# Optimization experiments

Measured on AMD Instinct MI355X. Metric: run time of the kernel, lower is better.

The kernel has to match this reference:

```python
import jax, jax.numpy as jnp
import numpy as np

N, C, H, W, NH = 2, 192, 256, 256, 6  # batch, channels, height, width, heads


def conv(x, w, groups=1):
    # NCHW conv, SAME padding, stride 1 (matches nn.Conv2d with padding=k//2)
    return jax.lax.conv_general_dilated(
        x, w, window_strides=(1, 1), padding='SAME',
        dimension_numbers=('NCHW', 'OIHW', 'NCHW'),
        feature_group_count=groups)


def setup_inputs() -> dict:
    key = jax.random.key(0)
    ks = jax.random.split(key, 5)
    x = jax.random.normal(ks[0], (N, C, H, W), jnp.float32)
    w1 = jax.random.normal(ks[1], (3 * C, C, 1, 1), jnp.float32) * 0.05   # 1x1 qkv proj
    w2 = jax.random.normal(ks[2], (3 * C, 1, 3, 3), jnp.float32) * 0.05   # depthwise 3x3
    w3 = jax.random.normal(ks[3], (3 * C, 1, 3, 3), jnp.float32) * 0.05   # depthwise 3x3
    factor = jnp.ones((1,), jnp.float32)                                   # learnable scale
    wf = jax.random.normal(ks[4], (C, C, 1, 1), jnp.float32) * 0.05       # final 1x1
    return {'x': x, 'w1': w1, 'w2': w2, 'w3': w3, 'factor': factor, 'wf': wf}


def reference(x, w1, w2, w3, factor, wf):
    n, c, h, w = x.shape
    dh = c // NH
    # conv-generated QKV: 1x1 -> depthwise 3x3 -> depthwise 3x3
    qkv = conv(conv(conv(x, w1), w2, groups=3 * c), w3, groups=3 * c)
    q, k, v = jnp.split(qkv, 3, axis=1)  # each [n, c, h, w]

    def rows(t):  # 'n (nh dh) h w -> (n nh h) w dh'  (row-wise axial attention)
        return t.reshape(n, NH, dh, h, w).transpose(0, 1, 3, 4, 2).reshape(n * NH * h, w, dh)

    q, k, v = rows(q), rows(k), rows(v)
    # L2-normalize along dh (F.normalize eps=1e-12 via clamp_min)
    q = q / jnp.maximum(jnp.linalg.norm(q, axis=-1, keepdims=True), 1e-12)
    k = k / jnp.maximum(jnp.linalg.norm(k, axis=-1, keepdims=True), 1e-12)
    scores = jnp.einsum('bqd,bkd->bqk', q, k) * factor[0]  # [(n nh h), w, w]
    attn = jax.nn.softmax(scores, axis=-1)
    out = jnp.einsum('bqk,bkd->bqd', attn, v)
    # '(n nh h) w dh -> n (nh dh) h w'
    out = out.reshape(n, NH, h, w, dh).transpose(0, 1, 4, 2, 3).reshape(n, c, h, w)
    return conv(out, wf)
```

## Files before the change

kernel.cpp:

```cpp
#include <hip/hip_runtime.h>
#include <hip/hip_bf16.h>
#include <math.h>

#define NB 2
#define CC 192
#define HH 256
#define WW 256
#define NHD 6
#define DH 32
#define C3 576

typedef __attribute__((ext_vector_type(8))) short bf16x8;
typedef __attribute__((ext_vector_type(4))) float f32x4;

__device__ __forceinline__ ushort f2b(float v) {
    __hip_bfloat16 b = __float2bfloat16(v);
    return *reinterpret_cast<ushort*>(&b);
}
__device__ __forceinline__ float b2f(ushort u) {
    __hip_bfloat16 b;
    *reinterpret_cast<ushort*>(&b) = u;
    return __bfloat162float(b);
}
__device__ __forceinline__ float bu(ushort u) {
    uint x = (uint)u << 16;
    return __uint_as_float(x);
}
__device__ __forceinline__ float exp2_fast(float x) {
#if __has_builtin(__builtin_amdgcn_exp2f)
    return __builtin_amdgcn_exp2f(x);
#else
    return exp2f(x);
#endif
}
__device__ __forceinline__ uint pk2(float x, float y) {
    return (__float_as_uint(y) & 0xFFFF0000u) | (__float_as_uint(x) >> 16);
}

__device__ __forceinline__ void gl_lds16(const void* g, void* l) {
    __builtin_amdgcn_global_load_lds((const __attribute__((address_space(1))) void*)g,
                                     (__attribute__((address_space(3))) void*)l, 16, 0, 0);
}

__global__ __launch_bounds__(256) void prep_w(const float* __restrict__ w1,
                                              const float* __restrict__ wf,
                                              ushort* __restrict__ Whi,
                                              ushort* __restrict__ Wlo) {
    int i = blockIdx.x * 256 + threadIdx.x;
    float v = (i < C3 * CC) ? w1[i] : wf[i - C3 * CC];
    ushort h = f2b(v);
    Whi[i] = h;
    Wlo[i] = f2b(v - b2f(h));
}

__global__ __launch_bounds__(256) void prep_xt(const float* __restrict__ x,
                                               ushort* __restrict__ Xhi,
                                               int n, int h0, int BH) {
    const int p0 = blockIdx.x * 64;
    const int gh = h0 - 2 + (p0 >> 8);
    const int wcol = p0 & 255;
    const int t = threadIdx.x;

    if (gh < 0 || gh >= HH) {
        uint* H = (uint*)(Xhi + (size_t)p0 * CC);
        for (int e = t; e < 64 * CC / 2; e += 256) H[e] = 0u;
        return;
    }

    __shared__ float xs[CC][65];
    const float* xb = x + ((size_t)n * CC) * (HH * WW) + (size_t)gh * WW + wcol;
    for (int e = t; e < CC * 16; e += 256) {
        int ic = e >> 4, j = e & 15;
        float4 v = *(const float4*)(xb + (size_t)ic * (HH * WW) + j * 4);
        xs[ic][j * 4 + 0] = v.x;
        xs[ic][j * 4 + 1] = v.y;
        xs[ic][j * 4 + 2] = v.z;
        xs[ic][j * 4 + 3] = v.w;
    }
    __syncthreads();

    const int r = t >> 2;
    const int k0 = (t & 3) * 48;
    uint* H = (uint*)(Xhi + ((size_t)p0 + r) * CC + k0);
    #pragma unroll
    for (int j = 0; j < 48; j += 2) {
        H[j >> 1] = (uint)f2b(xs[k0 + j][r]) | ((uint)f2b(xs[k0 + j + 1][r]) << 16);
    }
}

template<bool BSPLIT, bool OUTBF16>
__global__ __launch_bounds__(256) void gemm_split(const ushort* __restrict__ Whi,
                                                  const ushort* __restrict__ Wlo,
                                                  const ushort* __restrict__ Bhi,
                                                  const ushort* __restrict__ Blo,
                                                  void* __restrict__ Cout, int ldc,
                                                  int RS, int SS, int NM) {
    __shared__ ushort lA[2][64][64];
    __shared__ ushort lB[BSPLIT ? 2 : 1][128][64];

    const int bid = blockIdx.x;
    const int xcd = bid & 7;
    const int idx = bid >> 3;
    const int ptpx = (int)(gridDim.x >> 3) / NM;
    const int mtile = (idx % NM) * 64;
    const int ptile = (xcd * ptpx + idx / NM) * 128;

    const int t = threadIdx.x, wv = t >> 6, ln = t & 63;
    const int wm = wv >> 1, wn = wv & 1;

    f32x4 zero = {0.f, 0.f, 0.f, 0.f};
    f32x4 acc[2][4];
    #pragma unroll
    for (int fm = 0; fm < 2; ++fm)
        #pragma unroll
        for (int fn = 0; fn < 4; ++fn) acc[fm][fn] = zero;

    const int r8 = ln >> 3, s = ln & 7;
    const int CPW = BSPLIT ? 12 : 8;

    for (int kk = 0; kk < 3; ++kk) {
        const int k0 = kk * 64;
        #pragma unroll
        for (int ci = 0; ci < CPW; ++ci) {
            const int c = wv * CPW + ci;
            const ushort* g;
            void* l;
            if (c < 16) {
                const int pl = c >> 3, ch = c & 7;
                const int r = ch * 8 + r8;
                g = (pl ? Wlo : Whi) + (size_t)(mtile + r) * CC + k0 + ((s ^ (r & 7)) << 3);
                l = (void*)&lA[pl][ch * 8][0];
            } else {
                const int c2 = c - 16;
                const int pl = BSPLIT ? (c2 >> 4) : 0;
                const int ch = BSPLIT ? (c2 & 15) : c2;
                const int r = ch * 8 + r8;
                const int kq = k0 + ((s ^ (r & 7)) << 3);
                g = ((BSPLIT && pl) ? Blo : Bhi) + (size_t)(kq >> 5) * (size_t)SS
                                      + (size_t)(ptile + r) * (size_t)RS + (kq & 31);
                l = (void*)&lB[pl][ch * 8][0];
            }
            gl_lds16(g, l);
        }
        __syncthreads();

        #pragma unroll
        for (int ks = 0; ks < 2; ++ks) {
            bf16x8 ah[2], al[2], bh[4], bl[4];
            #pragma unroll
            for (int fm = 0; fm < 2; ++fm) {
                const int r = wm * 32 + fm * 16 + (ln & 15);
                const int col = (((ks * 4 + (ln >> 4)) ^ (r & 7)) << 3);
                ah[fm] = *(const bf16x8*)&lA[0][r][col];
                al[fm] = *(const bf16x8*)&lA[1][r][col];
            }
            #pragma unroll
            for (int fn = 0; fn < 4; ++fn) {
                const int r = wn * 64 + fn * 16 + (ln & 15);
                const int col = (((ks * 4 + (ln >> 4)) ^ (r & 7)) << 3);
                bh[fn] = *(const bf16x8*)&lB[0][r][col];
                if (BSPLIT) bl[fn] = *(const bf16x8*)&lB[1][r][col];
            }
            #pragma unroll
            for (int fm = 0; fm < 2; ++fm)
                #pragma unroll
                for (int fn = 0; fn < 4; ++fn) {
                    acc[fm][fn] = __builtin_amdgcn_mfma_f32_16x16x32_bf16(ah[fm], bh[fn], acc[fm][fn], 0, 0, 0);
                    if (BSPLIT)
                        acc[fm][fn] = __builtin_amdgcn_mfma_f32_16x16x32_bf16(ah[fm], bl[fn], acc[fm][fn], 0, 0, 0);
                    acc[fm][fn] = __builtin_amdgcn_mfma_f32_16x16x32_bf16(al[fm], bh[fn], acc[fm][fn], 0, 0, 0);
                }
        }
        __syncthreads();
    }

    #pragma unroll
    for (int fm = 0; fm < 2; ++fm)
        #pragma unroll
        for (int fn = 0; fn < 4; ++fn)
            #pragma unroll
            for (int r = 0; r < 4; ++r) {
                const int m = mtile + wm * 32 + fm * 16 + (ln >> 4) * 4 + r;
                const int p = ptile + wn * 64 + fn * 16 + (ln & 15);
                if (OUTBF16)
                    ((ushort*)Cout)[(size_t)m * ldc + p] = f2b(acc[fm][fn][r]);
                else
                    ((float*)Cout)[(size_t)m * ldc + p] = acc[fm][fn][r];
            }
}

struct RowH { float4 v; float l, r; };

__device__ __forceinline__ RowH k2_expand(ushort4 p, int ln) {
    RowH q;
    q.v = make_float4(bu(p.x), bu(p.y), bu(p.z), bu(p.w));
    q.l = __shfl_up(q.v.w, 1);
    q.r = __shfl_down(q.v.x, 1);
    if (ln == 0) q.l = 0.f;
    if (ln == 63) q.r = 0.f;
    return q;
}

__device__ __forceinline__ float4 k2_conv(const RowH& a, const RowH& b, const RowH& c,
                                          const float* w) {
    float4 o;
    o.x = fmaf(a.l,   w[0], fmaf(a.v.x, w[1], fmaf(a.v.y, w[2],
          fmaf(b.l,   w[3], fmaf(b.v.x, w[4], fmaf(b.v.y, w[5],
          fmaf(c.l,   w[6], fmaf(c.v.x, w[7], c.v.y * w[8]))))))));
    o.y = fmaf(a.v.x, w[0], fmaf(a.v.y, w[1], fmaf(a.v.z, w[2],
          fmaf(b.v.x, w[3], fmaf(b.v.y, w[4], fmaf(b.v.z, w[5],
          fmaf(c.v.x, w[6], fmaf(c.v.y, w[7], c.v.z * w[8]))))))));
    o.z = fmaf(a.v.y, w[0], fmaf(a.v.z, w[1], fmaf(a.v.w, w[2],
          fmaf(b.v.y, w[3], fmaf(b.v.z, w[4], fmaf(b.v.w, w[5],
          fmaf(c.v.y, w[6], fmaf(c.v.z, w[7], c.v.w * w[8]))))))));
    o.w = fmaf(a.v.z, w[0], fmaf(a.v.w, w[1], fmaf(a.r,   w[2],
          fmaf(b.v.z, w[3], fmaf(b.v.w, w[4], fmaf(b.r,   w[5],
          fmaf(c.v.z, w[6], fmaf(c.v.w, w[7], c.r * w[8]))))))));
    return o;
}

__device__ __forceinline__ RowH k2_mid(const RowH& a, const RowH& b, const RowH& c,
                                       const float* w, bool zero, int ln) {
    RowH m;
    if (zero) {
        m.v = make_float4(0.f, 0.f, 0.f, 0.f);
        m.l = 0.f; m.r = 0.f;
        return m;
    }
    m.v = k2_conv(a, b, c, w);
    m.l = __shfl_up(m.v.w, 1);
    m.r = __shfl_down(m.v.x, 1);
    if (ln == 0) m.l = 0.f;
    if (ln == 63) m.r = 0.f;
    return m;
}

__global__ __launch_bounds__(256) void k2_dwdw(const ushort* __restrict__ A,
                                               const float* __restrict__ w2,
                                               const float* __restrict__ w3,
                                               ushort* __restrict__ Bqk,
                                               float* __restrict__ Bv,
                                               int h0, int BH, int strips) {
    const int SR = BH / strips;
    const int wv = threadIdx.x >> 6, ln = threadIdx.x & 63;
    const int gid = blockIdx.x * 4 + wv;
    const int c = gid / strips;
    const int s = gid - c * strips;
    const int r0 = s * SR;

    float w2c[9], w3c[9];
    #pragma unroll
    for (int i = 0; i < 9; ++i) { w2c[i] = w2[c * 9 + i]; w3c[i] = w3[c * 9 + i]; }

    const ushort* Ac = A + (size_t)c * (BH + 4) * WW + 4 * ln;

    RowH i0 = k2_expand(*(const ushort4*)(Ac + (size_t)(r0 + 0) * WW), ln);
    RowH i1 = k2_expand(*(const ushort4*)(Ac + (size_t)(r0 + 1) * WW), ln);
    RowH i2 = k2_expand(*(const ushort4*)(Ac + (size_t)(r0 + 2) * WW), ln);
    ushort4 pf = *(const ushort4*)(Ac + (size_t)(r0 + 3) * WW);
    RowH m0 = k2_mid(i0, i1, i2, w2c, (h0 + r0 - 1) < 0, ln);
    i0 = i1; i1 = i2; i2 = k2_expand(pf, ln);
    pf = *(const ushort4*)(Ac + (size_t)(r0 + 4) * WW);
    RowH m1 = k2_mid(i0, i1, i2, w2c, false, ln);

    if (c < 2 * CC) {
        ushort* Bc = Bqk + (size_t)c * BH * WW + 4 * ln;
        #pragma unroll 4
        for (int r = r0; r < r0 + SR; ++r) {
            i0 = i1; i1 = i2; i2 = k2_expand(pf, ln);
            const int rn = (r + 5 < BH + 4) ? r + 5 : BH + 3;
            pf = *(const ushort4*)(Ac + (size_t)rn * WW);
            RowH m2 = k2_mid(i0, i1, i2, w2c, (h0 + r + 1) >= HH, ln);
            float4 o = k2_conv(m0, m1, m2, w3c);
            ushort4 ob;
            ob.x = f2b(o.x); ob.y = f2b(o.y); ob.z = f2b(o.z); ob.w = f2b(o.w);
            *(ushort4*)(Bc + (size_t)r * WW) = ob;
            m0 = m1; m1 = m2;
        }
    } else {
        float* Bc = Bv + (size_t)(c - 2 * CC) * BH * WW + 4 * ln;
        #pragma unroll 4
        for (int r = r0; r < r0 + SR; ++r) {
            i0 = i1; i1 = i2; i2 = k2_expand(pf, ln);
            const int rn = (r + 5 < BH + 4) ? r + 5 : BH + 3;
            pf = *(const ushort4*)(Ac + (size_t)rn * WW);
            RowH m2 = k2_mid(i0, i1, i2, w2c, (h0 + r + 1) >= HH, ln);
            float4 o = k2_conv(m0, m1, m2, w3c);
            *(float4*)(Bc + (size_t)r * WW) = o;
            m0 = m1; m1 = m2;
        }
    }
}

__global__ __launch_bounds__(512, 4) void k3_attn_mfma(const ushort* __restrict__ Bqk,
                                                       const float* __restrict__ Bv,
                                                       const float* __restrict__ factor,
                                                       ushort* __restrict__ Ohi,
                                                       ushort* __restrict__ Olo, int BH) {
    const int r = blockIdx.x / NHD;
    const int head = blockIdx.x % NHD;
    const int t = threadIdx.x;
    const size_t plane = (size_t)BH * WW;

    __shared__ __align__(16) char arena[49152];
    ushort* Ksp = (ushort*)arena;
    ushort* Vt  = (ushort*)(arena + 16384);
    uint*   Oar = (uint*)arena;

    const int wv = t >> 6, ln = t & 63;
    const int hig = ln >> 4, lo16 = ln & 15;
    const float fsc = factor[0];
    const float L2E = 1.4426950408889634f;
    const float mb2 = fabsf(fsc) * L2E;

    float qv[2][8];
    #pragma unroll
    for (int c = 0; c < 2; ++c) {
        const int qrow = wv * 32 + c * 16 + lo16;
        const ushort* qb = Bqk + ((size_t)(head * DH + hig * 8)) * plane + (size_t)r * WW + qrow;
        #pragma unroll
        for (int j = 0; j < 8; ++j) qv[c][j] = bu(qb[(size_t)j * plane]);
    }

    if (t < 256) {
        const int row = t;
        const ushort* base = Bqk + ((size_t)(CC + head * DH)) * plane + (size_t)r * WW + row;
        float v[32];
        #pragma unroll
        for (int d = 0; d < 32; ++d) v[d] = bu(base[(size_t)d * plane]);
        float ss = 0.f;
        #pragma unroll
        for (int d = 0; d < 32; ++d) ss = fmaf(v[d], v[d], ss);
        const float inv = 1.f / fmaxf(sqrtf(ss), 1e-12f);
        const int sw = (row >> 1) & 3;
        #pragma unroll
        for (int gq = 0; gq < 4; ++gq) {
            uint hu[4];
            #pragma unroll
            for (int j = 0; j < 4; ++j) {
                float v0 = v[gq * 8 + 2 * j] * inv, v1 = v[gq * 8 + 2 * j + 1] * inv;
                hu[j] = (uint)f2b(v0) | ((uint)f2b(v1) << 16);
            }
            const int off = row * 32 + ((gq ^ sw) << 3);
            *(uint4*)&Ksp[off] = make_uint4(hu[0], hu[1], hu[2], hu[3]);
        }
    } else {
        const int t2 = t - 256;
        const int kg = t2 & 63;
        const int d0 = (t2 >> 6) * 8;
        const int s_ = kg >> 3, b_ = (kg >> 2) & 1, g_ = kg & 3;
        const int kp4 = 32 * s_ + 8 * g_ + 4 * b_;
        const int slot = kp4 >> 3, inb = kp4 & 7;
        const float* base = Bv + ((size_t)(head * DH + d0)) * plane
                               + (size_t)r * WW + 4 * kg;
        #pragma unroll
        for (int jd = 0; jd < 8; ++jd) {
            const int d = d0 + jd;
            float4 vv = *(const float4*)(base + (size_t)jd * plane);
            ushort h0 = f2b(vv.x), h1 = f2b(vv.y), h2 = f2b(vv.z), h3 = f2b(vv.w);
            ushort l0 = f2b(vv.x - b2f(h0)), l1 = f2b(vv.y - b2f(h1));
            ushort l2 = f2b(vv.z - b2f(h2)), l3 = f2b(vv.w - b2f(h3));
            const int col = ((slot ^ (d & 7)) << 3) | inb;
            *(uint2*)&Vt[d * 256 + col] =
                make_uint2((uint)h0 | ((uint)h1 << 16), (uint)h2 | ((uint)h3 << 16));
            *(uint2*)&Vt[8192 + d * 256 + col] =
                make_uint2((uint)l0 | ((uint)l1 << 16), (uint)l2 | ((uint)l3 << 16));
        }
    }
    __syncthreads();

    union { bf16x8 v; uint u[4]; } qh_[2];
    #pragma unroll
    for (int c = 0; c < 2; ++c) {
        float ssq = 0.f;
        #pragma unroll
        for (int j = 0; j < 8; ++j) ssq = fmaf(qv[c][j], qv[c][j], ssq);
        ssq += __shfl_xor(ssq, 16);
        ssq += __shfl_xor(ssq, 32);
        const float qinv = fsc * L2E / fmaxf(sqrtf(ssq), 1e-12f);
        #pragma unroll
        for (int j = 0; j < 8; j += 2) {
            float v0 = qv[c][j] * qinv, v1 = qv[c][j + 1] * qinv;
            qh_[c].u[j >> 1] = (uint)f2b(v0) | ((uint)f2b(v1) << 16);
        }
    }

    f32x4 osave[2][2];
    float invl[2];

    #pragma unroll
    for (int c = 0; c < 2; ++c) {
        f32x4 s[16];
        const f32x4 cinit = {-mb2, -mb2, -mb2, -mb2};
        __builtin_amdgcn_s_setprio(1);
        #pragma unroll
        for (int f = 0; f < 16; ++f) {
            const int krow = f * 16 + lo16;
            const int koff = krow * 32 + ((hig ^ ((krow >> 1) & 3)) << 3);
            const bf16x8 kh = *(const bf16x8*)&Ksp[koff];
            s[f] = __builtin_amdgcn_mfma_f32_16x16x32_bf16(kh, qh_[c].v, cinit, 0, 0, 0);
        }
        __builtin_amdgcn_s_setprio(0);

        float lsum = 0.f;
        #pragma unroll
        for (int f = 0; f < 16; ++f) {
            #pragma unroll
            for (int rr = 0; rr < 4; ++rr) {
                float p = exp2_fast(s[f][rr]);
                s[f][rr] = p;
                lsum += p;
            }
        }
        lsum += __shfl_xor(lsum, 16);
        lsum += __shfl_xor(lsum, 32);
        invl[c] = 1.f / lsum;

        uint pu[32];
        #pragma unroll
        for (int f = 0; f < 16; ++f) {
            pu[2 * f]     = pk2(s[f][0], s[f][1]);
            pu[2 * f + 1] = pk2(s[f][2], s[f][3]);
        }

        f32x4 o0a = {0,0,0,0}, o0b = {0,0,0,0}, o1a = {0,0,0,0}, o1b = {0,0,0,0};
        __builtin_amdgcn_s_setprio(1);
        #pragma unroll
        for (int st = 0; st < 8; ++st) {
            union { bf16x8 v; uint u[4]; } pb;
            pb.u[0] = pu[4 * st];     pb.u[1] = pu[4 * st + 1];
            pb.u[2] = pu[4 * st + 2]; pb.u[3] = pu[4 * st + 3];
            {
                const int drow = lo16;
                const int voff = drow * 256 + (((4 * st + hig) ^ (drow & 7)) << 3);
                const bf16x8 vh = *(const bf16x8*)&Vt[voff];
                const bf16x8 vl = *(const bf16x8*)&Vt[8192 + voff];
                f32x4& o = (st & 1) ? o0b : o0a;
                o = __builtin_amdgcn_mfma_f32_16x16x32_bf16(vh, pb.v, o, 0, 0, 0);
                o = __builtin_amdgcn_mfma_f32_16x16x32_bf16(vl, pb.v, o, 0, 0, 0);
            }
            {
                const int drow = 16 + lo16;
                const int voff = drow * 256 + (((4 * st + hig) ^ (drow & 7)) << 3);
                const bf16x8 vh = *(const bf16x8*)&Vt[voff];
                const bf16x8 vl = *(const bf16x8*)&Vt[8192 + voff];
                f32x4& o = (st & 1) ? o1b : o1a;
                o = __builtin_amdgcn_mfma_f32_16x16x32_bf16(vh, pb.v, o, 0, 0, 0);
                o = __builtin_amdgcn_mfma_f32_16x16x32_bf16(vl, pb.v, o, 0, 0, 0);
            }
        }
        __builtin_amdgcn_s_setprio(0);
        #pragma unroll
        for (int rr = 0; rr < 4; ++rr) { o0a[rr] += o0b[rr]; o1a[rr] += o1b[rr]; }
        osave[c][0] = o0a;
        osave[c][1] = o1a;
    }

    __syncthreads();

    #pragma unroll
    for (int c = 0; c < 2; ++c) {
        const int qrow = wv * 32 + c * 16 + lo16;
        #pragma unroll
        for (int fm = 0; fm < 2; ++fm) {
            const f32x4 o = osave[c][fm];
            const float s0 = o[0] * invl[c], s1 = o[1] * invl[c];
            const float s2 = o[2] * invl[c], s3 = o[3] * invl[c];
            const ushort h0 = f2b(s0), h1 = f2b(s1), h2 = f2b(s2), h3 = f2b(s3);
            const ushort g0 = f2b(s0 - b2f(h0)), g1 = f2b(s1 - b2f(h1));
            const ushort g2 = f2b(s2 - b2f(h2)), g3 = f2b(s3 - b2f(h3));
            const int dp = 8 * fm + 2 * hig;
            Oar[qrow * 20 + dp]            = (uint)h0 | ((uint)h1 << 16);
            Oar[qrow * 20 + dp + 1]        = (uint)h2 | ((uint)h3 << 16);
            Oar[5120 + qrow * 20 + dp]     = (uint)g0 | ((uint)g1 << 16);
            Oar[5120 + qrow * 20 + dp + 1] = (uint)g2 | ((uint)g3 << 16);
        }
    }
    __syncthreads();

    if (t < 256) {
        const size_t obase = ((size_t)head * (size_t)BH * WW + (size_t)r * WW + t) * DH;
        uint4* dh_ = (uint4*)(Ohi + obase);
        uint4* dl_ = (uint4*)(Olo + obase);
        const uint* srcH = &Oar[t * 20];
        const uint* srcL = &Oar[5120 + t * 20];
        #pragma unroll
        for (int i = 0; i < 4; ++i) {
            dh_[i] = *(const uint4*)&srcH[i * 4];
            dl_[i] = *(const uint4*)&srcL[i * 4];
        }
    }
}

extern "C" void kernel_launch(void* const* d_in, const int* in_sizes, int n_in,
                              void* d_out, int out_size, void* d_ws, size_t ws_size,
                              hipStream_t stream) {
    const float* x      = (const float*)d_in[0];
    const float* w1     = (const float*)d_in[1];
    const float* w2     = (const float*)d_in[2];
    const float* w3     = (const float*)d_in[3];
    const float* factor = (const float*)d_in[4];
    const float* wf     = (const float*)d_in[5];
    float* out = (float*)d_out;

    const size_t SW = (size_t)(C3 + CC) * CC * 2 * sizeof(ushort);
    int BH = 256;
    while (BH > 32) {
        size_t SA_ = (size_t)C3 * (BH + 4) * WW * 2;
        size_t SB_ = (size_t)BH * WW * (2 * CC * 2 + CC * 4);
        size_t SO_ = (size_t)NHD * BH * WW * DH * 2 * 2;
        if (SA_ >= SO_ && SA_ + SB_ + SW <= ws_size) break;
        BH >>= 1;
    }
    const size_t SA = (size_t)C3 * (BH + 4) * WW * 2;
    const size_t SB = (size_t)BH * WW * (2 * CC * 2 + CC * 4);

    ushort* A   = (ushort*)d_ws;
    char*  Breg = (char*)d_ws + SA;
    ushort* Bqk = (ushort*)Breg;
    float*  Bv  = (float*)(Breg + (size_t)2 * CC * BH * WW * 2);
    ushort* Wsp = (ushort*)((char*)d_ws + SA + SB);
    ushort* Whi = Wsp;
    ushort* Wlo = Wsp + (size_t)(C3 + CC) * CC;

    ushort* Xhi = (ushort*)Breg;
    ushort* Ohi = A;
    ushort* Olo = Ohi + (size_t)NHD * BH * WW * DH;

    prep_w<<<dim3((C3 + CC) * CC / 256), dim3(256), 0, stream>>>(w1, wf, Whi, Wlo);

    for (int n = 0; n < NB; ++n) {
        for (int h0 = 0; h0 < HH; h0 += BH) {
            const int strips = BH / 16;
            prep_xt<<<dim3((BH + 4) * (WW / 64)), dim3(256), 0, stream>>>(x, Xhi, n, h0, BH);
            gemm_split<false, true><<<dim3(((BH + 4) * WW / 128) * (C3 / 64)), dim3(256), 0, stream>>>(
                Whi, Wlo, Xhi, nullptr, (void*)A, (BH + 4) * WW, CC, DH, C3 / 64);
            k2_dwdw<<<dim3(C3 * strips / 4), dim3(256), 0, stream>>>(A, w2, w3, Bqk, Bv, h0, BH, strips);
            k3_attn_mfma<<<dim3(NHD * BH), dim3(512), 0, stream>>>(Bqk, Bv, factor, Ohi, Olo, BH);
            gemm_split<true, false><<<dim3((BH * WW / 128) * (CC / 64)), dim3(256), 0, stream>>>(
                Whi + (size_t)C3 * CC, Wlo + (size_t)C3 * CC, Ohi, Olo,
                (void*)(out + ((size_t)n * CC) * HH * WW + (size_t)h0 * WW), HH * WW,
                DH, BH * WW * DH, CC / 64);
        }
    }
}
```

Baseline: 352.4 us.

## Store V and attention output as single bf16 instead of hi/lo split

V is now written by the depthwise kernel as bf16 in a pre-permuted column order, and the attention kernel loads it straight into LDS with direct global-to-LDS copies instead of converting fp32 into hi/lo bf16 pairs. The lo-part MFMAs for P·V are removed, the attention output is written as a single bf16 tensor, and the final 1x1 GEMM runs in single-activation mode. This cuts memory traffic, LDS footprint (allowing higher occupancy) and MFMA work, at the cost of lower precision on V and on the attention output.

```diff
diff --git a/kernel.cpp b/kernel.cpp
--- a/kernel.cpp
+++ b/kernel.cpp
@@ -239,7 +239,7 @@
                                                const float* __restrict__ w2,
                                                const float* __restrict__ w3,
                                                ushort* __restrict__ Bqk,
-                                               float* __restrict__ Bv,
+                                               ushort* __restrict__ Bvh,
                                                int h0, int BH, int strips) {
     const int SR = BH / strips;
     const int wv = threadIdx.x >> 6, ln = threadIdx.x & 63;
@@ -278,7 +278,8 @@
             m0 = m1; m1 = m2;
         }
     } else {
-        float* Bc = Bv + (size_t)(c - 2 * CC) * BH * WW + 4 * ln;
+        ushort* Bc = Bvh + (size_t)(c - 2 * CC) * BH * WW;
+        const int kp4 = 32 * (ln >> 3) + 8 * (ln & 3) + 4 * ((ln >> 2) & 1);
         #pragma unroll 4
         for (int r = r0; r < r0 + SR; ++r) {
             i0 = i1; i1 = i2; i2 = k2_expand(pf, ln);
@@ -286,23 +287,25 @@
             pf = *(const ushort4*)(Ac + (size_t)rn * WW);
             RowH m2 = k2_mid(i0, i1, i2, w2c, (h0 + r + 1) >= HH, ln);
             float4 o = k2_conv(m0, m1, m2, w3c);
-            *(float4*)(Bc + (size_t)r * WW) = o;
+            uint2 ob;
+            ob.x = (uint)f2b(o.x) | ((uint)f2b(o.y) << 16);
+            ob.y = (uint)f2b(o.z) | ((uint)f2b(o.w) << 16);
+            *(uint2*)(Bc + (size_t)r * WW + kp4) = ob;
             m0 = m1; m1 = m2;
         }
     }
 }
 
 __global__ __launch_bounds__(512, 4) void k3_attn_mfma(const ushort* __restrict__ Bqk,
-                                                       const float* __restrict__ Bv,
+                                                       const ushort* __restrict__ Bvh,
                                                        const float* __restrict__ factor,
-                                                       ushort* __restrict__ Ohi,
-                                                       ushort* __restrict__ Olo, int BH) {
+                                                       ushort* __restrict__ Ohi, int BH) {
     const int r = blockIdx.x / NHD;
     const int head = blockIdx.x % NHD;
     const int t = threadIdx.x;
     const size_t plane = (size_t)BH * WW;
 
-    __shared__ __align__(16) char arena[49152];
+    __shared__ __align__(16) char arena[32768];
     ushort* Ksp = (ushort*)arena;
     ushort* Vt  = (ushort*)(arena + 16384);
     uint*   Oar = (uint*)arena;
@@ -312,6 +315,15 @@
     const float fsc = factor[0];
     const float L2E = 1.4426950408889634f;
     const float mb2 = fabsf(fsc) * L2E;
+
+    #pragma unroll
+    for (int it = 0; it < 2; ++it) {
+        const int G = (wv * 2 + it) * 64 + ln;
+        const int d = G >> 5, g = G & 31;
+        const ushort* src = Bvh + ((size_t)(head * DH + d) * BH + r) * WW
+                                + ((g ^ (d & 7)) << 3);
+        gl_lds16(src, (void*)(Vt + (size_t)(wv * 2 + it) * 512));
+    }
 
     float qv[2][8];
     #pragma unroll
@@ -343,28 +355,6 @@
             }
             const int off = row * 32 + ((gq ^ sw) << 3);
             *(uint4*)&Ksp[off] = make_uint4(hu[0], hu[1], hu[2], hu[3]);
-        }
-    } else {
-        const int t2 = t - 256;
-        const int kg = t2 & 63;
-        const int d0 = (t2 >> 6) * 8;
-        const int s_ = kg >> 3, b_ = (kg >> 2) & 1, g_ = kg & 3;
-        const int kp4 = 32 * s_ + 8 * g_ + 4 * b_;
-        const int slot = kp4 >> 3, inb = kp4 & 7;
-        const float* base = Bv + ((size_t)(head * DH + d0)) * plane
-                               + (size_t)r * WW + 4 * kg;
-        #pragma unroll
-        for (int jd = 0; jd < 8; ++jd) {
-            const int d = d0 + jd;
-            float4 vv = *(const float4*)(base + (size_t)jd * plane);
-            ushort h0 = f2b(vv.x), h1 = f2b(vv.y), h2 = f2b(vv.z), h3 = f2b(vv.w);
-            ushort l0 = f2b(vv.x - b2f(h0)), l1 = f2b(vv.y - b2f(h1));
-            ushort l2 = f2b(vv.z - b2f(h2)), l3 = f2b(vv.w - b2f(h3));
-            const int col = ((slot ^ (d & 7)) << 3) | inb;
-            *(uint2*)&Vt[d * 256 + col] =
-                make_uint2((uint)h0 | ((uint)h1 << 16), (uint)h2 | ((uint)h3 << 16));
-            *(uint2*)&Vt[8192 + d * 256 + col] =
-                make_uint2((uint)l0 | ((uint)l1 << 16), (uint)l2 | ((uint)l3 << 16));
         }
     }
     __syncthreads();
@@ -434,19 +424,15 @@
                 const int drow = lo16;
                 const int voff = drow * 256 + (((4 * st + hig) ^ (drow & 7)) << 3);
                 const bf16x8 vh = *(const bf16x8*)&Vt[voff];
-                const bf16x8 vl = *(const bf16x8*)&Vt[8192 + voff];
                 f32x4& o = (st & 1) ? o0b : o0a;
                 o = __builtin_amdgcn_mfma_f32_16x16x32_bf16(vh, pb.v, o, 0, 0, 0);
-                o = __builtin_amdgcn_mfma_f32_16x16x32_bf16(vl, pb.v, o, 0, 0, 0);
             }
             {
                 const int drow = 16 + lo16;
                 const int voff = drow * 256 + (((4 * st + hig) ^ (drow & 7)) << 3);
                 const bf16x8 vh = *(const bf16x8*)&Vt[voff];
-                const bf16x8 vl = *(const bf16x8*)&Vt[8192 + voff];
                 f32x4& o = (st & 1) ? o1b : o1a;
                 o = __builtin_amdgcn_mfma_f32_16x16x32_bf16(vh, pb.v, o, 0, 0, 0);
-                o = __builtin_amdgcn_mfma_f32_16x16x32_bf16(vl, pb.v, o, 0, 0, 0);
             }
         }
         __builtin_amdgcn_s_setprio(0);
@@ -466,14 +452,9 @@
             const f32x4 o = osave[c][fm];
             const float s0 = o[0] * invl[c], s1 = o[1] * invl[c];
             const float s2 = o[2] * invl[c], s3 = o[3] * invl[c];
-            const ushort h0 = f2b(s0), h1 = f2b(s1), h2 = f2b(s2), h3 = f2b(s3);
-            const ushort g0 = f2b(s0 - b2f(h0)), g1 = f2b(s1 - b2f(h1));
-            const ushort g2 = f2b(s2 - b2f(h2)), g3 = f2b(s3 - b2f(h3));
             const int dp = 8 * fm + 2 * hig;
-            Oar[qrow * 20 + dp]            = (uint)h0 | ((uint)h1 << 16);
-            Oar[qrow * 20 + dp + 1]        = (uint)h2 | ((uint)h3 << 16);
-            Oar[5120 + qrow * 20 + dp]     = (uint)g0 | ((uint)g1 << 16);
-            Oar[5120 + qrow * 20 + dp + 1] = (uint)g2 | ((uint)g3 << 16);
+            Oar[qrow * 20 + dp]     = (uint)f2b(s0) | ((uint)f2b(s1) << 16);
+            Oar[qrow * 20 + dp + 1] = (uint)f2b(s2) | ((uint)f2b(s3) << 16);
         }
     }
     __syncthreads();
@@ -481,14 +462,9 @@
     if (t < 256) {
         const size_t obase = ((size_t)head * (size_t)BH * WW + (size_t)r * WW + t) * DH;
         uint4* dh_ = (uint4*)(Ohi + obase);
-        uint4* dl_ = (uint4*)(Olo + obase);
         const uint* srcH = &Oar[t * 20];
-        const uint* srcL = &Oar[5120 + t * 20];
-        #pragma unroll
-        for (int i = 0; i < 4; ++i) {
-            dh_[i] = *(const uint4*)&srcH[i * 4];
-            dl_[i] = *(const uint4*)&srcL[i * 4];
-        }
+        #pragma unroll
+        for (int i = 0; i < 4; ++i) dh_[i] = *(const uint4*)&srcH[i * 4];
     }
 }
 
@@ -507,25 +483,25 @@
     int BH = 256;
     while (BH > 32) {
         size_t SA_ = (size_t)C3 * (BH + 4) * WW * 2;
-        size_t SB_ = (size_t)BH * WW * (2 * CC * 2 + CC * 4);
-        size_t SO_ = (size_t)NHD * BH * WW * DH * 2 * 2;
-        if (SA_ >= SO_ && SA_ + SB_ + SW <= ws_size) break;
+        size_t SB_ = (size_t)BH * WW * C3 * 2;
+        size_t SX_ = (size_t)(BH + 4) * WW * CC * 2;
+        size_t SO_ = (size_t)NHD * BH * WW * DH * 2;
+        if (SA_ >= SO_ && SB_ >= SX_ && SA_ + SB_ + SW <= ws_size) break;
         BH >>= 1;
     }
     const size_t SA = (size_t)C3 * (BH + 4) * WW * 2;
-    const size_t SB = (size_t)BH * WW * (2 * CC * 2 + CC * 4);
+    const size_t SB = (size_t)BH * WW * C3 * 2;
 
     ushort* A   = (ushort*)d_ws;
     char*  Breg = (char*)d_ws + SA;
     ushort* Bqk = (ushort*)Breg;
-    float*  Bv  = (float*)(Breg + (size_t)2 * CC * BH * WW * 2);
+    ushort* Bvh = (ushort*)(Breg + (size_t)2 * CC * BH * WW * 2);
     ushort* Wsp = (ushort*)((char*)d_ws + SA + SB);
     ushort* Whi = Wsp;
     ushort* Wlo = Wsp + (size_t)(C3 + CC) * CC;
 
     ushort* Xhi = (ushort*)Breg;
     ushort* Ohi = A;
-    ushort* Olo = Ohi + (size_t)NHD * BH * WW * DH;
 
     prep_w<<<dim3((C3 + CC) * CC / 256), dim3(256), 0, stream>>>(w1, wf, Whi, Wlo);
 
@@ -535,10 +511,10 @@
             prep_xt<<<dim3((BH + 4) * (WW / 64)), dim3(256), 0, stream>>>(x, Xhi, n, h0, BH);
             gemm_split<false, true><<<dim3(((BH + 4) * WW / 128) * (C3 / 64)), dim3(256), 0, stream>>>(
                 Whi, Wlo, Xhi, nullptr, (void*)A, (BH + 4) * WW, CC, DH, C3 / 64);
-            k2_dwdw<<<dim3(C3 * strips / 4), dim3(256), 0, stream>>>(A, w2, w3, Bqk, Bv, h0, BH, strips);
-            k3_attn_mfma<<<dim3(NHD * BH), dim3(512), 0, stream>>>(Bqk, Bv, factor, Ohi, Olo, BH);
-            gemm_split<true, false><<<dim3((BH * WW / 128) * (CC / 64)), dim3(256), 0, stream>>>(
-                Whi + (size_t)C3 * CC, Wlo + (size_t)C3 * CC, Ohi, Olo,
+            k2_dwdw<<<dim3(C3 * strips / 4), dim3(256), 0, stream>>>(A, w2, w3, Bqk, Bvh, h0, BH, strips);
+            k3_attn_mfma<<<dim3(NHD * BH), dim3(512), 0, stream>>>(Bqk, Bvh, factor, Ohi, BH);
+            gemm_split<false, false><<<dim3((BH * WW / 128) * (CC / 64)), dim3(256), 0, stream>>>(
+                Whi + (size_t)C3 * CC, Wlo + (size_t)C3 * CC, Ohi, nullptr,
                 (void*)(out + ((size_t)n * CC) * HH * WW + (size_t)h0 * WW), HH * WW,
                 DH, BH * WW * DH, CC / 64);
         }
```

After: 321.3 us. -8.8%, faster.
